# Kernel tuning notes

Measured on AMD Instinct MI355X. Metric: run time of the kernel, lower is better.

## Reference

```python
import jax, jax.numpy as jnp
import numpy as np

B, S, D = 2, 2048, 1024
H, HD = 16, 64

def setup_inputs() -> dict:
    key = jax.random.key(0)
    k1, k2, k3, k4 = jax.random.split(key, 4)
    inputs = jax.random.normal(k1, (B, S, D), dtype=jnp.float32)
    scale = 1.0 / np.sqrt(D)
    Wq = jax.random.normal(k2, (D, H * HD), dtype=jnp.float32) * scale
    Wk = jax.random.normal(k3, (D, H * HD), dtype=jnp.float32) * scale
    Wv = jax.random.normal(k4, (D, H * HD), dtype=jnp.float32) * scale
    return {"inputs": inputs, "Wq": Wq, "Wk": Wk, "Wv": Wv}

def _split_heads(x):
    # [B,S,H*HD] -> [B,H,S,HD]; tf.split along last axis == reshape then transpose
    b, s, _ = x.shape
    return x.reshape(b, s, H, HD).transpose(0, 2, 1, 3)

def reference(inputs, Wq, Wk, Wv):
    q = _split_heads(inputs @ Wq)  # [B,H,S,HD]
    k = _split_heads(inputs @ Wk)
    v = _split_heads(inputs @ Wv)
    scores = jnp.einsum("bhsd,bhtd->bhst", q, k) / jnp.sqrt(jnp.float32(HD))
    attn = jax.nn.softmax(scores, axis=-1)  # [B,H,S,S]
    out = jnp.einsum("bhst,bhtd->bhsd", attn, v)  # [B,H,S,HD]
    # concat heads back: [B,S,H*HD]
    return out.transpose(0, 2, 1, 3).reshape(inputs.shape[0], inputs.shape[1], H * HD)
```

## Files before the change

### kernel.cpp

```cpp
#include <hip/hip_runtime.h>

typedef __attribute__((ext_vector_type(8))) short short8;
typedef __attribute__((ext_vector_type(4))) float f32x4;
typedef __attribute__((ext_vector_type(16))) float f32x16;

#define B_  2
#define S_  2048
#define D_  1024
#define H_  16
#define HD_ 64
#define M_  (B_*S_)
#define N_  (H_*HD_)
#define HSZ ((size_t)B_*H_*S_*HD_)

#define QSCALE 0.18033688011112042f

__device__ __forceinline__ unsigned short f2bf(float f) {
  unsigned int u = __float_as_uint(f);
  u += 0x7fffu + ((u >> 16) & 1u);
  return (unsigned short)(u >> 16);
}

__device__ __forceinline__ unsigned int cvt_pk_bf16(float lo, float hi) {
  unsigned int r;
  asm("v_cvt_pk_bf16_f32 %0, %1, %2" : "=v"(r) : "v"(lo), "v"(hi));
  return r;
}

__device__ __forceinline__ float exp2_fast(float x) {
  float r;
  asm("v_exp_f32 %0, %1" : "=v"(r) : "v"(x));
  return r;
}

__device__ __forceinline__ void gll16(const void* g, void* l) {
  __builtin_amdgcn_global_load_lds(
      (const __attribute__((address_space(1))) void*)g,
      (__attribute__((address_space(3))) void*)l, 16, 0, 0);
}

__global__ void cvt_x_kernel(const float* __restrict__ x, unsigned short* __restrict__ xb) {
  int i = blockIdx.x * blockDim.x + threadIdx.x;
  float4 v = reinterpret_cast<const float4*>(x)[i];
  ushort4 o;
  o.x = f2bf(v.x); o.y = f2bf(v.y); o.z = f2bf(v.z); o.w = f2bf(v.w);
  reinterpret_cast<ushort4*>(xb)[i] = o;
}

__global__ void cvt_w_transpose_kernel(const float* __restrict__ w0, const float* __restrict__ w1,
                                       const float* __restrict__ w2, unsigned short* __restrict__ wt) {
  __shared__ float tile[32][33];
  const float* w = blockIdx.z == 0 ? w0 : (blockIdx.z == 1 ? w1 : w2);
  unsigned short* o = wt + (size_t)blockIdx.z * D_ * N_;
  int kbase = blockIdx.y * 32, nbase = blockIdx.x * 32;
#pragma unroll
  for (int i = 0; i < 4; i++)
    tile[threadIdx.y + i*8][threadIdx.x] =
        w[(size_t)(kbase + threadIdx.y + i*8) * N_ + nbase + threadIdx.x];
  __syncthreads();
#pragma unroll
  for (int i = 0; i < 4; i++)
    o[(size_t)(nbase + threadIdx.y + i*8) * D_ + kbase + threadIdx.x] =
        f2bf(tile[threadIdx.x][threadIdx.y + i*8]);
}

__global__ __launch_bounds__(256) void qkv_gemm_kernel(const unsigned short* __restrict__ xb,
                                                       const unsigned short* __restrict__ wt,
                                                       unsigned short* __restrict__ qkv) {
  __shared__ __align__(16) unsigned short As[128 * 64];
  __shared__ __align__(16) unsigned short Bs[128 * 64];
  const unsigned short* w = wt + (size_t)blockIdx.z * D_ * N_;
  unsigned short* out = qkv + (size_t)blockIdx.z * HSZ;
  int lane = threadIdx.x & 63, wave = threadIdx.x >> 6;
  int lr = lane & 15, lk = lane >> 4;
  int mblk = blockIdx.y * 128, nblk = blockIdx.x * 128;
  int wm = (wave >> 1) * 64, wn = (wave & 1) * 64;

  int srow0 = wave * 32 + (lane >> 3);
  int scol = lane & 7;
  f32x4 acc[4][4] = {};

  for (int kk = 0; kk < D_; kk += 64) {
    __syncthreads();
#pragma unroll
    for (int it = 0; it < 4; it++) {
      int row = srow0 + it * 8;
      int ce = (scol ^ (row & 7)) * 8;
      gll16(xb + (size_t)(mblk + row) * D_ + kk + ce,
            (void*)(As + (size_t)(wave * 4 + it) * 512));
      gll16(w  + (size_t)(nblk + row) * D_ + kk + ce,
            (void*)(Bs + (size_t)(wave * 4 + it) * 512));
    }
    __syncthreads();

    short8 a[2][4], b[2][4];
#pragma unroll
    for (int i = 0; i < 4; i++) {
      int row = wm + i * 16 + lr;
      const char* rp = (const char*)As + row * 128;
#pragma unroll
      for (int ks = 0; ks < 2; ks++)
        a[ks][i] = *reinterpret_cast<const short8*>(rp + ((((ks*4 + lk) ^ (row & 7))) << 4));
    }
#pragma unroll
    for (int j = 0; j < 4; j++) {
      int row = wn + j * 16 + lr;
      const char* rp = (const char*)Bs + row * 128;
#pragma unroll
      for (int ks = 0; ks < 2; ks++)
        b[ks][j] = *reinterpret_cast<const short8*>(rp + ((((ks*4 + lk) ^ (row & 7))) << 4));
    }
#pragma unroll
    for (int ks = 0; ks < 2; ks++)
#pragma unroll
      for (int i = 0; i < 4; i++)
#pragma unroll
        for (int j = 0; j < 4; j++)
          acc[i][j] = __builtin_amdgcn_mfma_f32_16x16x32_bf16(a[ks][i], b[ks][j], acc[i][j], 0, 0, 0);
  }

  if (blockIdx.z == 2) {
#pragma unroll
    for (int i = 0; i < 4; i++) {
      int m0 = mblk + wm + i*16 + lk*4;
      int bb = m0 >> 11, s0 = m0 & (S_-1);
#pragma unroll
      for (int j = 0; j < 4; j++) {
        int n = nblk + wn + j*16 + lr;
        int h = n >> 6, d = n & (HD_-1);
        ushort4 pk;
        pk.x = f2bf(acc[i][j][0]); pk.y = f2bf(acc[i][j][1]);
        pk.z = f2bf(acc[i][j][2]); pk.w = f2bf(acc[i][j][3]);
        *reinterpret_cast<ushort4*>(out + ((size_t)(bb*H_ + h)*HD_ + d)*S_ + s0) = pk;
      }
    }
  } else {
    float qs = (blockIdx.z == 0) ? QSCALE : 1.0f;
#pragma unroll
    for (int i = 0; i < 4; i++)
#pragma unroll
      for (int j = 0; j < 4; j++)
#pragma unroll
        for (int r = 0; r < 4; r++) {
          int m = mblk + wm + i*16 + lk*4 + r;
          int n = nblk + wn + j*16 + lr;
          int bb = m >> 11, s = m & (S_-1), h = n >> 6, d = n & (HD_-1);
          out[(((size_t)bb * H_ + h) * S_ + s) * HD_ + d] = f2bf(acc[i][j][r] * qs);
        }
  }
}

__global__ __launch_bounds__(256) void attn_kernel(const unsigned short* __restrict__ qkv,
                                                   float* __restrict__ out) {
  int hid = blockIdx.x;
  int wrk = (hid & 7) * 64 + (hid >> 3);
  int bh = wrk >> 4, qtile = wrk & 15;

  const unsigned short* Q  = qkv +            (size_t)bh * S_ * HD_;
  const unsigned short* K  = qkv + HSZ   +    (size_t)bh * S_ * HD_;
  const unsigned short* Vt = qkv + 2*HSZ +    (size_t)bh * HD_ * S_;
  int lane = threadIdx.x & 63, wave = threadIdx.x >> 6;
  int ql = lane & 31, hi = lane >> 5;
  int qbase = qtile * 128 + wave * 32;

  __shared__ __align__(16) unsigned short Ks[2][64 * 64];
  __shared__ __align__(16) unsigned short Vs[2][64 * 64];

  int tid = threadIdx.x;

  short8 qf[4];
#pragma unroll
  for (int ds = 0; ds < 4; ds++)
    qf[ds] = *reinterpret_cast<const short8*>(Q + (size_t)(qbase + ql) * HD_ + ds*16 + hi*8);

  f32x16 oacc[2] = {};
  float m = -INFINITY, lsum = 0.f;

#pragma unroll
  for (int it = 0; it < 2; it++) {
    int ci = it * 256 + tid, row = ci >> 3, c = ci & 7;
    int ce = (c ^ (row & 7)) * 8;
    gll16(K  + (size_t)row * HD_ + ce, (void*)(Ks[0] + (size_t)ci * 8));
    gll16(Vt + (size_t)row * S_  + ce, (void*)(Vs[0] + (size_t)ci * 8));
  }

  int buf = 0;
  for (int kt = 0; kt < S_/64; kt++) {
    __syncthreads();
    if (kt < S_/64 - 1) {
      int kc1 = (kt + 1) * 64;
#pragma unroll
      for (int it = 0; it < 2; it++) {
        int ci = it * 256 + tid, row = ci >> 3, c = ci & 7;
        int ce = (c ^ (row & 7)) * 8;
        gll16(K  + (size_t)(kc1 + row) * HD_ + ce, (void*)(Ks[buf^1] + (size_t)ci * 8));
        gll16(Vt + (size_t)row * S_ + kc1 + ce,    (void*)(Vs[buf^1] + (size_t)ci * 8));
      }
    }

    f32x16 sacc[2] = {};
    __builtin_amdgcn_s_setprio(1);
#pragma unroll
    for (int kh = 0; kh < 2; kh++) {
      int row = kh*32 + ql;
      const char* rp = (const char*)Ks[buf] + row * 128;
#pragma unroll
      for (int ds = 0; ds < 4; ds++) {
        short8 kf = *reinterpret_cast<const short8*>(rp + (((ds*2 + hi) ^ (row & 7)) << 4));
        sacc[kh] = __builtin_amdgcn_mfma_f32_32x32x16_bf16(kf, qf[ds], sacc[kh], 0, 0, 0);
      }
    }
    __builtin_amdgcn_s_setprio(0);

    float tm[16];
#pragma unroll
    for (int r = 0; r < 16; r++) tm[r] = fmaxf(sacc[0][r], sacc[1][r]);
#pragma unroll
    for (int st = 8; st > 0; st >>= 1)
#pragma unroll
      for (int r = 0; r < st; r++) tm[r] = fmaxf(tm[r], tm[r + st]);
    float mx = fmaxf(tm[0], __shfl_xor(tm[0], 32));
    if (__any(mx - m > 8.0f)) {
      float mnew = fmaxf(m, mx);
      float corr = exp2_fast(m - mnew);
      m = mnew;
      lsum *= corr;
#pragma unroll
      for (int dh = 0; dh < 2; dh++)
#pragma unroll
        for (int r = 0; r < 16; r++) oacc[dh][r] *= corr;
    }
#pragma unroll
    for (int kh = 0; kh < 2; kh++)
#pragma unroll
      for (int r = 0; r < 16; r++)
        sacc[kh][r] = exp2_fast(sacc[kh][r] - m);
    float ts[16];
#pragma unroll
    for (int r = 0; r < 16; r++) ts[r] = sacc[0][r] + sacc[1][r];
#pragma unroll
    for (int st = 8; st > 0; st >>= 1)
#pragma unroll
      for (int r = 0; r < st; r++) ts[r] += ts[r + st];
    lsum += ts[0] + __shfl_xor(ts[0], 32);

#pragma unroll
    for (int ks = 0; ks < 4; ks++) {
      int o = (ks & 1) * 8;
      unsigned int w0, w1, w2, w3;
      if (ks < 2) {
        w0 = cvt_pk_bf16(sacc[0][o+0], sacc[0][o+1]);
        w1 = cvt_pk_bf16(sacc[0][o+2], sacc[0][o+3]);
        w2 = cvt_pk_bf16(sacc[0][o+4], sacc[0][o+5]);
        w3 = cvt_pk_bf16(sacc[0][o+6], sacc[0][o+7]);
      } else {
        w0 = cvt_pk_bf16(sacc[1][o+0], sacc[1][o+1]);
        w1 = cvt_pk_bf16(sacc[1][o+2], sacc[1][o+3]);
        w2 = cvt_pk_bf16(sacc[1][o+4], sacc[1][o+5]);
        w3 = cvt_pk_bf16(sacc[1][o+6], sacc[1][o+7]);
      }
      asm("v_permlane32_swap_b32 %0, %1" : "+v"(w0), "+v"(w2));
      asm("v_permlane32_swap_b32 %0, %1" : "+v"(w1), "+v"(w3));
      union { unsigned int u[4]; short8 s; } pf;
      pf.u[0] = w0; pf.u[1] = w1; pf.u[2] = w2; pf.u[3] = w3;
      __builtin_amdgcn_s_setprio(1);
#pragma unroll
      for (int dh = 0; dh < 2; dh++) {
        int row = dh*32 + ql;
        short8 vf = *reinterpret_cast<const short8*>(
            (const char*)Vs[buf] + row * 128 + (((ks*2 + hi) ^ (row & 7)) << 4));
        oacc[dh] = __builtin_amdgcn_mfma_f32_32x32x16_bf16(vf, pf.s, oacc[dh], 0, 0, 0);
      }
      __builtin_amdgcn_s_setprio(0);
    }
    buf ^= 1;
  }

  float inv = 1.0f / lsum;
  int b0 = bh >> 4, h = bh & (H_-1);
  int s = qbase + ql;
  float* orow = out + ((size_t)b0 * S_ + s) * N_ + h * HD_;
#pragma unroll
  for (int dh = 0; dh < 2; dh++)
#pragma unroll
    for (int a = 0; a < 4; a++) {
      float4 vv;
      vv.x = oacc[dh][a*4+0] * inv; vv.y = oacc[dh][a*4+1] * inv;
      vv.z = oacc[dh][a*4+2] * inv; vv.w = oacc[dh][a*4+3] * inv;
      *reinterpret_cast<float4*>(orow + dh*32 + 8*a + 4*hi) = vv;
    }
}

extern "C" void kernel_launch(void* const* d_in, const int* in_sizes, int n_in,
                              void* d_out, int out_size, void* d_ws, size_t ws_size,
                              hipStream_t stream) {
  const float* X  = (const float*)d_in[0];
  const float* Wq = (const float*)d_in[1];
  const float* Wk = (const float*)d_in[2];
  const float* Wv = (const float*)d_in[3];
  float* out = (float*)d_out;

  unsigned short* Xb  = (unsigned short*)d_ws;
  unsigned short* Wt  = Xb + (size_t)M_ * D_;
  unsigned short* QKV = Wt + (size_t)3 * D_ * N_;

  cvt_x_kernel<<<(M_*D_)/(256*4), 256, 0, stream>>>(X, Xb);
  cvt_w_transpose_kernel<<<dim3(N_/32, D_/32, 3), dim3(32, 8), 0, stream>>>(Wq, Wk, Wv, Wt);
  qkv_gemm_kernel<<<dim3(N_/128, M_/128, 3), 256, 0, stream>>>(Xb, Wt, QKV);
  attn_kernel<<<(S_/128) * (B_*H_), 256, 0, stream>>>(QKV, out);
}
```

Baseline: 123.4 us.

## Widen attention KV tile to 128 and compute row sums via MFMA

The attention kernel now stages 128 keys per iteration instead of 64, which halves the loop trip count and the number of barriers and max/rescale passes. The LDS swizzle is extended to cover the larger tiles. The softmax row sum is no longer a VALU tree reduction plus cross-lane shuffle; it is computed by an extra MFMA that multiplies the bf16 probabilities by a vector of ones. This adds matrix-core work, doubles the LDS footprint per block and raises register pressure, and the sum is now taken over bf16-rounded probabilities.

New measurement: 140.2 us. 1.14x slower.

```diff
diff --git a/kernel.cpp b/kernel.cpp
--- a/kernel.cpp
+++ b/kernel.cpp
@@ -162,51 +162,56 @@
   int lane = threadIdx.x & 63, wave = threadIdx.x >> 6;
   int ql = lane & 31, hi = lane >> 5;
   int qbase = qtile * 128 + wave * 32;
-
-  __shared__ __align__(16) unsigned short Ks[2][64 * 64];
-  __shared__ __align__(16) unsigned short Vs[2][64 * 64];
-
   int tid = threadIdx.x;
+
+  __shared__ __align__(16) unsigned short Ks[2][128 * 64];
+  __shared__ __align__(16) unsigned short Vs[2][64 * 128];
+
+#define STAGE(b, kc) do {                                                        \
+    _Pragma("unroll")                                                            \
+    for (int it = 0; it < 4; it++) {                                             \
+      int ci = it * 256 + tid;                                                   \
+      int kr = ci >> 3, kcol = ci & 7;                                           \
+      gll16(K + (size_t)((kc) + kr) * HD_ +                                      \
+                ((kcol ^ (kr & 7) ^ ((kr >> 3) & 7)) * 8),                       \
+            (void*)(Ks[b] + (size_t)ci * 8));                                    \
+      int vr = ci >> 4, vcol = ci & 15;                                          \
+      gll16(Vt + (size_t)vr * S_ + (kc) +                                        \
+                 ((vcol ^ (vr & 7) ^ ((vr >> 3) & 7)) * 8),                      \
+            (void*)(Vs[b] + (size_t)ci * 8));                                    \
+    }                                                                            \
+  } while (0)
 
   short8 qf[4];
 #pragma unroll
   for (int ds = 0; ds < 4; ds++)
     qf[ds] = *reinterpret_cast<const short8*>(Q + (size_t)(qbase + ql) * HD_ + ds*16 + hi*8);
 
+  short8 ones;
+#pragma unroll
+  for (int i = 0; i < 8; i++) ones[i] = (short)0x3F80;
+
   f32x16 oacc[2] = {};
-  float m = -INFINITY, lsum = 0.f;
-
-#pragma unroll
-  for (int it = 0; it < 2; it++) {
-    int ci = it * 256 + tid, row = ci >> 3, c = ci & 7;
-    int ce = (c ^ (row & 7)) * 8;
-    gll16(K  + (size_t)row * HD_ + ce, (void*)(Ks[0] + (size_t)ci * 8));
-    gll16(Vt + (size_t)row * S_  + ce, (void*)(Vs[0] + (size_t)ci * 8));
-  }
+  f32x16 lacc = {};
+  float m = -INFINITY;
+
+  STAGE(0, 0);
 
   int buf = 0;
-  for (int kt = 0; kt < S_/64; kt++) {
+  for (int kt = 0; kt < S_/128; kt++) {
     __syncthreads();
-    if (kt < S_/64 - 1) {
-      int kc1 = (kt + 1) * 64;
-#pragma unroll
-      for (int it = 0; it < 2; it++) {
-        int ci = it * 256 + tid, row = ci >> 3, c = ci & 7;
-        int ce = (c ^ (row & 7)) * 8;
-        gll16(K  + (size_t)(kc1 + row) * HD_ + ce, (void*)(Ks[buf^1] + (size_t)ci * 8));
-        gll16(Vt + (size_t)row * S_ + kc1 + ce,    (void*)(Vs[buf^1] + (size_t)ci * 8));
-      }
-    }
-
-    f32x16 sacc[2] = {};
+    if (kt < S_/128 - 1) STAGE(buf^1, (kt+1)*128);
+
+    f32x16 sacc[4] = {};
     __builtin_amdgcn_s_setprio(1);
 #pragma unroll
-    for (int kh = 0; kh < 2; kh++) {
+    for (int kh = 0; kh < 4; kh++) {
       int row = kh*32 + ql;
       const char* rp = (const char*)Ks[buf] + row * 128;
+      int sw = (row & 7) ^ ((row >> 3) & 7);
 #pragma unroll
       for (int ds = 0; ds < 4; ds++) {
-        short8 kf = *reinterpret_cast<const short8*>(rp + (((ds*2 + hi) ^ (row & 7)) << 4));
+        short8 kf = *reinterpret_cast<const short8*>(rp + (((ds*2 + hi) ^ sw) << 4));
         sacc[kh] = __builtin_amdgcn_mfma_f32_32x32x16_bf16(kf, qf[ds], sacc[kh], 0, 0, 0);
       }
     }
@@ -214,7 +219,8 @@
 
     float tm[16];
 #pragma unroll
-    for (int r = 0; r < 16; r++) tm[r] = fmaxf(sacc[0][r], sacc[1][r]);
+    for (int r = 0; r < 16; r++)
+      tm[r] = fmaxf(fmaxf(sacc[0][r], sacc[1][r]), fmaxf(sacc[2][r], sacc[3][r]));
 #pragma unroll
     for (int st = 8; st > 0; st >>= 1)
 #pragma unroll
@@ -224,51 +230,37 @@
       float mnew = fmaxf(m, mx);
       float corr = exp2_fast(m - mnew);
       m = mnew;
-      lsum *= corr;
+      lacc[0] *= corr;
 #pragma unroll
       for (int dh = 0; dh < 2; dh++)
 #pragma unroll
         for (int r = 0; r < 16; r++) oacc[dh][r] *= corr;
     }
 #pragma unroll
-    for (int kh = 0; kh < 2; kh++)
+    for (int kh = 0; kh < 4; kh++)
 #pragma unroll
       for (int r = 0; r < 16; r++)
         sacc[kh][r] = exp2_fast(sacc[kh][r] - m);
-    float ts[16];
-#pragma unroll
-    for (int r = 0; r < 16; r++) ts[r] = sacc[0][r] + sacc[1][r];
-#pragma unroll
-    for (int st = 8; st > 0; st >>= 1)
-#pragma unroll
-      for (int r = 0; r < st; r++) ts[r] += ts[r + st];
-    lsum += ts[0] + __shfl_xor(ts[0], 32);
-
-#pragma unroll
-    for (int ks = 0; ks < 4; ks++) {
+
+#pragma unroll
+    for (int ks = 0; ks < 8; ks++) {
       int o = (ks & 1) * 8;
-      unsigned int w0, w1, w2, w3;
-      if (ks < 2) {
-        w0 = cvt_pk_bf16(sacc[0][o+0], sacc[0][o+1]);
-        w1 = cvt_pk_bf16(sacc[0][o+2], sacc[0][o+3]);
-        w2 = cvt_pk_bf16(sacc[0][o+4], sacc[0][o+5]);
-        w3 = cvt_pk_bf16(sacc[0][o+6], sacc[0][o+7]);
-      } else {
-        w0 = cvt_pk_bf16(sacc[1][o+0], sacc[1][o+1]);
-        w1 = cvt_pk_bf16(sacc[1][o+2], sacc[1][o+3]);
-        w2 = cvt_pk_bf16(sacc[1][o+4], sacc[1][o+5]);
-        w3 = cvt_pk_bf16(sacc[1][o+6], sacc[1][o+7]);
-      }
+      unsigned int w0 = cvt_pk_bf16(sacc[ks>>1][o+0], sacc[ks>>1][o+1]);
+      unsigned int w1 = cvt_pk_bf16(sacc[ks>>1][o+2], sacc[ks>>1][o+3]);
+      unsigned int w2 = cvt_pk_bf16(sacc[ks>>1][o+4], sacc[ks>>1][o+5]);
+      unsigned int w3 = cvt_pk_bf16(sacc[ks>>1][o+6], sacc[ks>>1][o+7]);
       asm("v_permlane32_swap_b32 %0, %1" : "+v"(w0), "+v"(w2));
       asm("v_permlane32_swap_b32 %0, %1" : "+v"(w1), "+v"(w3));
       union { unsigned int u[4]; short8 s; } pf;
       pf.u[0] = w0; pf.u[1] = w1; pf.u[2] = w2; pf.u[3] = w3;
       __builtin_amdgcn_s_setprio(1);
+      lacc = __builtin_amdgcn_mfma_f32_32x32x16_bf16(ones, pf.s, lacc, 0, 0, 0);
 #pragma unroll
       for (int dh = 0; dh < 2; dh++) {
         int row = dh*32 + ql;
+        int sw = (row & 7) ^ ((row >> 3) & 7);
         short8 vf = *reinterpret_cast<const short8*>(
-            (const char*)Vs[buf] + row * 128 + (((ks*2 + hi) ^ (row & 7)) << 4));
+            (const char*)Vs[buf] + row * 256 + (((ks*2 + hi) ^ sw) << 4));
         oacc[dh] = __builtin_amdgcn_mfma_f32_32x32x16_bf16(vf, pf.s, oacc[dh], 0, 0, 0);
       }
       __builtin_amdgcn_s_setprio(0);
@@ -276,7 +268,7 @@
     buf ^= 1;
   }
 
-  float inv = 1.0f / lsum;
+  float inv = 1.0f / lacc[0];
   int b0 = bh >> 4, h = bh & (H_-1);
   int s = qbase + ql;
   float* orow = out + ((size_t)b0 * S_ + s) * N_ + h * HD_;
@@ -289,6 +281,7 @@
       vv.z = oacc[dh][a*4+2] * inv; vv.w = oacc[dh][a*4+3] * inv;
       *reinterpret_cast<float4*>(orow + dh*32 + 8*a + 4*hi) = vv;
     }
+#undef STAGE
 }
 
 extern "C" void kernel_launch(void* const* d_in, const int* in_sizes, int n_in,
```
